# Performance work log

Hardware: AMD Instinct MI355X
Metric: run time of the kernel (lower is better)

## Reference

```python
import jax, jax.numpy as jnp
import numpy as np
from jax import lax

B, CIN, H, W = 32, 128, 64, 64
COUT, K, NK, HID = 128, 3, 4, 32
TEMP = 34.0
PAD = 1


def setup_inputs() -> dict:
    key = jax.random.key(0)
    k1, k2, k3, k4 = jax.random.split(key, 4)
    x = jax.random.normal(k1, (B, CIN, H, W), dtype=jnp.float32)
    fc1_w = jax.random.normal(k2, (HID, CIN), dtype=jnp.float32) * (2.0 / CIN) ** 0.5
    fc2_w = jax.random.normal(k3, (NK, HID), dtype=jnp.float32) * (2.0 / HID) ** 0.5
    fc2_b = jnp.zeros((NK,), dtype=jnp.float32)
    weight = jax.random.normal(k4, (NK, COUT, CIN, K, K), dtype=jnp.float32) * 0.05
    bias = jnp.zeros((NK, COUT), dtype=jnp.float32)
    return {"x": x, "fc1_w": fc1_w, "fc2_w": fc2_w, "fc2_b": fc2_b,
            "weight": weight, "bias": bias}


def _per_sample_conv(xi, wi):
    # xi: [CIN, H, W], wi: [COUT, CIN, K, K]
    out = lax.conv_general_dilated(
        xi[None], wi,
        window_strides=(1, 1),
        padding=[(PAD, PAD), (PAD, PAD)],
        dimension_numbers=("NCHW", "OIHW", "NCHW"))
    return out[0]  # [COUT, H', W']


def reference(x, fc1_w, fc2_w, fc2_b, weight, bias):
    # attention: global avg pool -> 1x1 conv (matmul) -> relu -> 1x1 conv -> softmax
    context = jnp.mean(x, axis=(2, 3))                      # [B, CIN]
    hid = jax.nn.relu(context @ fc1_w.T)                    # [B, HID]
    logits = hid @ fc2_w.T + fc2_b                          # [B, NK]
    att = jax.nn.softmax(logits / TEMP, axis=1)             # [B, NK]
    # aggregate per-sample kernels and biases
    agg_w = jnp.einsum("bk,koihw->boihw", att, weight)      # [B, COUT, CIN, K, K]
    agg_b = att @ bias                                      # [B, COUT]
    # per-sample convolution (equivalent to the groups=B trick in torch)
    out = jax.vmap(_per_sample_conv)(x, agg_w)              # [B, COUT, H, W]
    return out + agg_b[:, :, None, None]
```

## Files before the change

### kernel.cpp

```cpp
#include <hip/hip_runtime.h>

#define B_    32
#define CIN_  128
#define H_    64
#define W_    64
#define COUT_ 128
#define NK_   4
#define HID_  32
#define TEMP_ 34.0f

typedef short bf16x8 __attribute__((ext_vector_type(8)));
typedef float f32x16 __attribute__((ext_vector_type(16)));

__device__ __forceinline__ short f2bf(float f) {
    union { float f; unsigned u; } c; c.f = f;
    unsigned r = (c.u + 0x7FFFu + ((c.u >> 16) & 1u)) >> 16;
    return (short)r;
}

__global__ __launch_bounds__(64) void k_context(const float* __restrict__ x,
                                                float* __restrict__ ctx) {
    const int bc = blockIdx.x;
    const float* p = x + (size_t)bc * (H_ * W_);
    const int lane = threadIdx.x;
    float s = 0.f;
    for (int i = lane * 4; i < H_ * W_; i += 64 * 4) {
        float4 v = *(const float4*)(p + i);
        s += v.x + v.y + v.z + v.w;
    }
    for (int off = 32; off > 0; off >>= 1) s += __shfl_down(s, off, 64);
    if (lane == 0) ctx[bc] = s * (1.0f / (H_ * W_));
}

__global__ __launch_bounds__(256) void k_aggw(const float* __restrict__ ctx,
        const float* __restrict__ fc1w, const float* __restrict__ fc2w,
        const float* __restrict__ fc2b, const float* __restrict__ bias,
        const float* __restrict__ weight, short* __restrict__ aggwt,
        float* __restrict__ aggb) {
    __shared__ float hidp[8][32];
    __shared__ float shid[32];
    __shared__ float satt[NK_];
    const int tid = threadIdx.x;
    const int blk = blockIdx.x;
    const int b = blk >> 6;
    {
        const int hh = tid & 31, part = tid >> 5;
        const float* c  = ctx + b * CIN_ + part * 16;
        const float* f1 = fc1w + hh * CIN_ + part * 16;
        float s = 0.f;
#pragma unroll
        for (int j = 0; j < 16; ++j) s += c[j] * f1[j];
        hidp[part][hh] = s;
    }
    __syncthreads();
    if (tid < 32) {
        float s = 0.f;
#pragma unroll
        for (int p = 0; p < 8; ++p) s += hidp[p][tid];
        shid[tid] = fmaxf(s, 0.f);
    }
    __syncthreads();
    if (tid == 0) {
        float lg[NK_]; float mx = -1e30f;
#pragma unroll
        for (int k = 0; k < NK_; ++k) {
            float s = fc2b[k];
            for (int hh = 0; hh < HID_; ++hh) s += shid[hh] * fc2w[k * HID_ + hh];
            lg[k] = s / TEMP_; mx = fmaxf(mx, lg[k]);
        }
        float den = 0.f;
#pragma unroll
        for (int k = 0; k < NK_; ++k) { lg[k] = expf(lg[k] - mx); den += lg[k]; }
        const float rd = 1.0f / den;
#pragma unroll
        for (int k = 0; k < NK_; ++k) satt[k] = lg[k] * rd;
    }
    __syncthreads();
    const float a0 = satt[0], a1 = satt[1], a2 = satt[2], a3 = satt[3];

    const int idx = blk * 256 + tid;
    const int ci = idx & 127;
    const int co = (idx >> 7) & 127;
    if ((tid & 127) == 0)
        aggb[b * COUT_ + co] = a0 * bias[co] + a1 * bias[COUT_ + co]
                             + a2 * bias[2 * COUT_ + co] + a3 * bias[3 * COUT_ + co];

    const float* w0 = weight + ((size_t)co * CIN_ + ci) * 9;
    const float* w1 = w0 + (size_t)COUT_ * CIN_ * 9;
    const float* w2 = w1 + (size_t)COUT_ * CIN_ * 9;
    const float* w3 = w2 + (size_t)COUT_ * CIN_ * 9;
    short* o = aggwt + ((size_t)(b * COUT_ + co) * 9) * CIN_ + ci;
#pragma unroll
    for (int r = 0; r < 9; ++r)
        o[r * CIN_] = f2bf(a0 * w0[r] + a1 * w1[r] + a2 * w2[r] + a3 * w3[r]);
}

#define RBY 8448
#define RSH 4224
__global__ __launch_bounds__(256, 2) void k_conv(const float* __restrict__ x,
        const short* __restrict__ aggwt, const float* __restrict__ aggb,
        float* __restrict__ out) {
    __shared__ short xt[6 * RSH];
    const int tid = threadIdx.x;
    const int blk = blockIdx.x;
    const int b = blk & 31;
    const int h0 = (blk >> 5) * 4;
    const int lane = tid & 63;
    const int wv = tid >> 6;
    const int l31 = lane & 31;
    const int lane5 = lane >> 5;

    if (tid < 96) {
        const int row = tid >> 4;
        const int q = tid & 15;
        const int cl = (q < 8) ? q : (512 + q);
        *(int4*)(&xt[row * RSH + cl * 8]) = make_int4(0, 0, 0, 0);
    }

    f32x16 acc[8];
#pragma unroll
    for (int t = 0; t < 8; ++t)
#pragma unroll
        for (int k = 0; k < 16; ++k) acc[t][k] = 0.f;

    const short* Ap = aggwt + (size_t)(b * COUT_ + wv * 32 + l31) * 9 * CIN_ + lane5 * 8;

    for (int half = 0; half < 2; ++half) {
        const int cib = half * 64;
#pragma unroll
        for (int k = 0; k < 12; ++k) {
            const int task = k * 4 + wv;
            const int row = task >> 3;
            const int g = task & 7;
            const int in_h = h0 - 1 + row;
            bf16x8 v = (bf16x8){0, 0, 0, 0, 0, 0, 0, 0};
            if (in_h >= 0 && in_h < H_) {
                const float* gp = x + (((size_t)b * CIN_ + cib + g * 8) * H_ + in_h) * W_ + lane;
                float f[8];
#pragma unroll
                for (int j = 0; j < 8; ++j) f[j] = gp[j * (H_ * W_)];
#pragma unroll
                for (int j = 0; j < 8; ++j) v[j] = f2bf(f[j]);
            }
            *(bf16x8*)(&xt[row * RSH + ((lane + 1) * 8 + ((g + lane) & 7)) * 8]) = v;
        }
        __syncthreads();

#pragma unroll
        for (int kcl = 0; kcl < 4; ++kcl) {
            const int kc = half * 4 + kcl;
            bf16x8 av[9];
#pragma unroll
            for (int r = 0; r < 9; ++r)
                av[r] = *(const bf16x8*)(Ap + kc * 16 + r * CIN_);
#pragma unroll
            for (int ir = 0; ir < 6; ++ir) {
                bf16x8 bv[2][3];
#pragma unroll
                for (int i = 0; i < 2; ++i)
#pragma unroll
                    for (int kw = 0; kw < 3; ++kw) {
                        const int s = i * 32 + l31 + kw;
                        const int off = 16 * ((2 * kcl + lane5 + s - 1) & 7);
                        bv[i][kw] = *(const bf16x8*)((const char*)xt + ir * RBY + s * 128 + off);
                    }
#pragma unroll
                for (int orr = 0; orr < 4; ++orr) {
                    if (orr <= ir && ir <= orr + 2) {
                        const int kh = ir - orr;
#pragma unroll
                        for (int i = 0; i < 2; ++i)
#pragma unroll
                            for (int kw = 0; kw < 3; ++kw)
                                acc[orr * 2 + i] = __builtin_amdgcn_mfma_f32_32x32x16_bf16(
                                    av[kh * 3 + kw], bv[i][kw], acc[orr * 2 + i], 0, 0, 0);
                    }
                }
            }
        }
        if (half == 0) __syncthreads();
    }

    const float* ab = aggb + b * COUT_;
#pragma unroll
    for (int orr = 0; orr < 4; ++orr) {
#pragma unroll
        for (int i = 0; i < 2; ++i) {
            const int hh = h0 + orr;
            const int w = i * 32 + l31;
            float* op = out + ((size_t)b * COUT_ * H_ + hh) * W_ + w;
            const f32x16 a = acc[orr * 2 + i];
#pragma unroll
            for (int reg = 0; reg < 16; ++reg) {
                const int co = wv * 32 + (reg & 3) + 8 * (reg >> 2) + 4 * lane5;
                op[(size_t)co * (H_ * W_)] = a[reg] + ab[co];
            }
        }
    }
}

extern "C" void kernel_launch(void* const* d_in, const int* in_sizes, int n_in,
                              void* d_out, int out_size, void* d_ws, size_t ws_size,
                              hipStream_t stream) {
    const float* x    = (const float*)d_in[0];
    const float* fc1w = (const float*)d_in[1];
    const float* fc2w = (const float*)d_in[2];
    const float* fc2b = (const float*)d_in[3];
    const float* wgt  = (const float*)d_in[4];
    const float* bias = (const float*)d_in[5];
    float* out = (float*)d_out;

    char* ws = (char*)d_ws;
    float* ctx   = (float*)(ws + 0);
    float* aggb  = (float*)(ws + 16384);
    short* aggwt = (short*)(ws + 65536);

    k_context<<<dim3(B_ * CIN_), dim3(64), 0, stream>>>(x, ctx);
    k_aggw<<<dim3((B_ * COUT_ * CIN_) / 256), dim3(256), 0, stream>>>(
        ctx, fc1w, fc2w, fc2b, bias, wgt, aggwt, aggb);
    k_conv<<<dim3(B_ * (H_ / 4)), dim3(256), 0, stream>>>(x, aggwt, aggb, out);
}
```

Baseline: 171.2 us.

## Split conv tiles by width halves and coalesce aggregated-weight writes via LDS

The conv kernel now gives each block a 32-wide half of the image row, so each block has half the accumulators and half the LDS tile, and the grid doubles. Launch bounds rise to 3 blocks per CU for more occupancy. In exchange, each block reloads the 34-wide input window including halo columns, and A-fragment loads are repeated across the two width halves. The weight aggregation kernel now processes two output channels per block, reading float4 weights and transposing through shared memory so the bf16 stores are 16-byte writes instead of scattered 2-byte ones.

After: 191.9 us. 12.0% more time.

```diff
diff --git a/kernel.cpp b/kernel.cpp
--- a/kernel.cpp
+++ b/kernel.cpp
@@ -40,11 +40,13 @@
     __shared__ float hidp[8][32];
     __shared__ float shid[32];
     __shared__ float satt[NK_];
-    const int tid = threadIdx.x;
+    __shared__ float sbuf[2304];
+    const int t = threadIdx.x;
     const int blk = blockIdx.x;
     const int b = blk >> 6;
+    const int co0 = (blk & 63) * 2;
     {
-        const int hh = tid & 31, part = tid >> 5;
+        const int hh = t & 31, part = t >> 5;
         const float* c  = ctx + b * CIN_ + part * 16;
         const float* f1 = fc1w + hh * CIN_ + part * 16;
         float s = 0.f;
@@ -53,14 +55,14 @@
         hidp[part][hh] = s;
     }
     __syncthreads();
-    if (tid < 32) {
+    if (t < 32) {
         float s = 0.f;
 #pragma unroll
-        for (int p = 0; p < 8; ++p) s += hidp[p][tid];
-        shid[tid] = fmaxf(s, 0.f);
-    }
-    __syncthreads();
-    if (tid == 0) {
+        for (int p = 0; p < 8; ++p) s += hidp[p][t];
+        shid[t] = fmaxf(s, 0.f);
+    }
+    __syncthreads();
+    if (t == 0) {
         float lg[NK_]; float mx = -1e30f;
 #pragma unroll
         for (int k = 0; k < NK_; ++k) {
@@ -78,48 +80,69 @@
     __syncthreads();
     const float a0 = satt[0], a1 = satt[1], a2 = satt[2], a3 = satt[3];
 
-    const int idx = blk * 256 + tid;
-    const int ci = idx & 127;
-    const int co = (idx >> 7) & 127;
-    if ((tid & 127) == 0)
+    if ((t & 127) == 0) {
+        const int co = co0 + (t >> 7);
         aggb[b * COUT_ + co] = a0 * bias[co] + a1 * bias[COUT_ + co]
                              + a2 * bias[2 * COUT_ + co] + a3 * bias[3 * COUT_ + co];
-
-    const float* w0 = weight + ((size_t)co * CIN_ + ci) * 9;
-    const float* w1 = w0 + (size_t)COUT_ * CIN_ * 9;
-    const float* w2 = w1 + (size_t)COUT_ * CIN_ * 9;
-    const float* w3 = w2 + (size_t)COUT_ * CIN_ * 9;
-    short* o = aggwt + ((size_t)(b * COUT_ + co) * 9) * CIN_ + ci;
-#pragma unroll
-    for (int r = 0; r < 9; ++r)
-        o[r * CIN_] = f2bf(a0 * w0[r] + a1 * w1[r] + a2 * w2[r] + a3 * w3[r]);
-}
-
-#define RBY 8448
-#define RSH 4224
-__global__ __launch_bounds__(256, 2) void k_conv(const float* __restrict__ x,
+    }
+
+    const size_t kstride = (size_t)COUT_ * CIN_ * 9;
+    const float* W0 = weight + (size_t)co0 * (CIN_ * 9);
+#pragma unroll
+    for (int jj = 0; jj < 3; ++jj) {
+        const int i4 = jj * 256 + t;
+        if (i4 < 576) {
+            const float4 w0 = *(const float4*)(W0 + i4 * 4);
+            const float4 w1 = *(const float4*)(W0 + kstride + i4 * 4);
+            const float4 w2 = *(const float4*)(W0 + 2 * kstride + i4 * 4);
+            const float4 w3 = *(const float4*)(W0 + 3 * kstride + i4 * 4);
+            float4 r;
+            r.x = a0 * w0.x + a1 * w1.x + a2 * w2.x + a3 * w3.x;
+            r.y = a0 * w0.y + a1 * w1.y + a2 * w2.y + a3 * w3.y;
+            r.z = a0 * w0.z + a1 * w1.z + a2 * w2.z + a3 * w3.z;
+            r.w = a0 * w0.w + a1 * w1.w + a2 * w2.w + a3 * w3.w;
+            *(float4*)(&sbuf[i4 * 4]) = r;
+        }
+    }
+    __syncthreads();
+#pragma unroll
+    for (int jj = 0; jj < 2; ++jj) {
+        const int g = jj * 256 + t;
+        if (g < 288) {
+            const int coL = (g >= 144) ? 1 : 0;
+            const int gg = g - coL * 144;
+            const int r  = gg >> 4;
+            const int oc = gg & 15;
+            bf16x8 v;
+#pragma unroll
+            for (int e = 0; e < 8; ++e)
+                v[e] = f2bf(sbuf[(coL * 128 + oc * 8 + e) * 9 + r]);
+            short* dst = aggwt + ((size_t)(b * COUT_ + co0 + coL) * 9 + r) * CIN_ + oc * 8;
+            *(bf16x8*)dst = v;
+        }
+    }
+}
+
+#define RBY2 4352
+#define RSH2 2176
+__global__ __launch_bounds__(256, 3) void k_conv(const float* __restrict__ x,
         const short* __restrict__ aggwt, const float* __restrict__ aggb,
         float* __restrict__ out) {
-    __shared__ short xt[6 * RSH];
+    __shared__ short xt[6 * RSH2];
     const int tid = threadIdx.x;
     const int blk = blockIdx.x;
     const int b = blk & 31;
-    const int h0 = (blk >> 5) * 4;
+    const int rest = blk >> 5;
+    const int h0 = (rest >> 1) * 4;
+    const int iw = rest & 1;
     const int lane = tid & 63;
     const int wv = tid >> 6;
     const int l31 = lane & 31;
     const int lane5 = lane >> 5;
 
-    if (tid < 96) {
-        const int row = tid >> 4;
-        const int q = tid & 15;
-        const int cl = (q < 8) ? q : (512 + q);
-        *(int4*)(&xt[row * RSH + cl * 8]) = make_int4(0, 0, 0, 0);
-    }
-
-    f32x16 acc[8];
-#pragma unroll
-    for (int t = 0; t < 8; ++t)
+    f32x16 acc[4];
+#pragma unroll
+    for (int t = 0; t < 4; ++t)
 #pragma unroll
         for (int k = 0; k < 16; ++k) acc[t][k] = 0.f;
 
@@ -133,16 +156,19 @@
             const int row = task >> 3;
             const int g = task & 7;
             const int in_h = h0 - 1 + row;
-            bf16x8 v = (bf16x8){0, 0, 0, 0, 0, 0, 0, 0};
-            if (in_h >= 0 && in_h < H_) {
-                const float* gp = x + (((size_t)b * CIN_ + cib + g * 8) * H_ + in_h) * W_ + lane;
-                float f[8];
-#pragma unroll
-                for (int j = 0; j < 8; ++j) f[j] = gp[j * (H_ * W_)];
-#pragma unroll
-                for (int j = 0; j < 8; ++j) v[j] = f2bf(f[j]);
+            if (lane < 34) {
+                const int w = iw * 32 - 1 + lane;
+                bf16x8 v = (bf16x8){0, 0, 0, 0, 0, 0, 0, 0};
+                if (in_h >= 0 && in_h < H_ && w >= 0 && w < W_) {
+                    const float* gp = x + (((size_t)b * CIN_ + cib + g * 8) * H_ + in_h) * W_ + w;
+                    float f[8];
+#pragma unroll
+                    for (int j = 0; j < 8; ++j) f[j] = gp[j * (H_ * W_)];
+#pragma unroll
+                    for (int j = 0; j < 8; ++j) v[j] = f2bf(f[j]);
+                }
+                *(bf16x8*)(&xt[row * RSH2 + lane * 64 + ((g + lane - 1) & 7) * 8]) = v;
             }
-            *(bf16x8*)(&xt[row * RSH + ((lane + 1) * 8 + ((g + lane) & 7)) * 8]) = v;
         }
         __syncthreads();
 
@@ -155,25 +181,21 @@
                 av[r] = *(const bf16x8*)(Ap + kc * 16 + r * CIN_);
 #pragma unroll
             for (int ir = 0; ir < 6; ++ir) {
-                bf16x8 bv[2][3];
-#pragma unroll
-                for (int i = 0; i < 2; ++i)
-#pragma unroll
-                    for (int kw = 0; kw < 3; ++kw) {
-                        const int s = i * 32 + l31 + kw;
-                        const int off = 16 * ((2 * kcl + lane5 + s - 1) & 7);
-                        bv[i][kw] = *(const bf16x8*)((const char*)xt + ir * RBY + s * 128 + off);
-                    }
+                bf16x8 bv[3];
+#pragma unroll
+                for (int kw = 0; kw < 3; ++kw) {
+                    const int s = l31 + kw;
+                    const int off = 16 * ((2 * kcl + lane5 + s - 1) & 7);
+                    bv[kw] = *(const bf16x8*)((const char*)xt + ir * RBY2 + s * 128 + off);
+                }
 #pragma unroll
                 for (int orr = 0; orr < 4; ++orr) {
                     if (orr <= ir && ir <= orr + 2) {
                         const int kh = ir - orr;
 #pragma unroll
-                        for (int i = 0; i < 2; ++i)
-#pragma unroll
-                            for (int kw = 0; kw < 3; ++kw)
-                                acc[orr * 2 + i] = __builtin_amdgcn_mfma_f32_32x32x16_bf16(
-                                    av[kh * 3 + kw], bv[i][kw], acc[orr * 2 + i], 0, 0, 0);
+                        for (int kw = 0; kw < 3; ++kw)
+                            acc[orr] = __builtin_amdgcn_mfma_f32_32x32x16_bf16(
+                                av[kh * 3 + kw], bv[kw], acc[orr], 0, 0, 0);
                     }
                 }
             }
@@ -184,17 +206,14 @@
     const float* ab = aggb + b * COUT_;
 #pragma unroll
     for (int orr = 0; orr < 4; ++orr) {
-#pragma unroll
-        for (int i = 0; i < 2; ++i) {
-            const int hh = h0 + orr;
-            const int w = i * 32 + l31;
-            float* op = out + ((size_t)b * COUT_ * H_ + hh) * W_ + w;
-            const f32x16 a = acc[orr * 2 + i];
-#pragma unroll
-            for (int reg = 0; reg < 16; ++reg) {
-                const int co = wv * 32 + (reg & 3) + 8 * (reg >> 2) + 4 * lane5;
-                op[(size_t)co * (H_ * W_)] = a[reg] + ab[co];
-            }
+        const int hh = h0 + orr;
+        const int w = iw * 32 + l31;
+        float* op = out + ((size_t)b * COUT_ * H_ + hh) * W_ + w;
+        const f32x16 a = acc[orr];
+#pragma unroll
+        for (int reg = 0; reg < 16; ++reg) {
+            const int co = wv * 32 + (reg & 3) + 8 * (reg >> 2) + 4 * lane5;
+            op[(size_t)co * (H_ * W_)] = a[reg] + ab[co];
         }
     }
 }
@@ -216,7 +235,7 @@
     short* aggwt = (short*)(ws + 65536);
 
     k_context<<<dim3(B_ * CIN_), dim3(64), 0, stream>>>(x, ctx);
-    k_aggw<<<dim3((B_ * COUT_ * CIN_) / 256), dim3(256), 0, stream>>>(
+    k_aggw<<<dim3(B_ * (COUT_ / 2)), dim3(256), 0, stream>>>(
         ctx, fc1w, fc2w, fc2b, bias, wgt, aggwt, aggb);
-    k_conv<<<dim3(B_ * (H_ / 4)), dim3(256), 0, stream>>>(x, aggwt, aggb, out);
-}
+    k_conv<<<dim3(B_ * (H_ / 4) * 2), dim3(256), 0, stream>>>(x, aggwt, aggb, out);
+}
```
